# Performance work log

Hardware: AMD Instinct MI355X
Metric: run time of the kernel (lower is better)

Reference implementation:

```python
import jax, jax.numpy as jnp
import numpy as np

N_NODES = 100000
N_EDGES = 1600000
IN_F, HID_F, OUT_F = 64, 64, 64


def setup_inputs() -> dict:
    key = jax.random.key(0)
    ks = jax.random.split(key, 9)
    return {
        "x": jax.random.normal(ks[0], (N_NODES, IN_F), dtype=jnp.float32),
        "src": jax.random.randint(ks[1], (N_EDGES,), 0, N_NODES, dtype=jnp.int64),
        "dst": jax.random.randint(ks[2], (N_EDGES,), 0, N_NODES, dtype=jnp.int64),
        "W_self1": jax.random.normal(ks[3], (IN_F, HID_F), dtype=jnp.float32) * (1.0 / np.sqrt(IN_F)),
        "W_neigh1": jax.random.normal(ks[4], (IN_F, HID_F), dtype=jnp.float32) * (1.0 / np.sqrt(IN_F)),
        "b1": jnp.zeros((HID_F,), dtype=jnp.float32),
        "W_self2": jax.random.normal(ks[5], (HID_F, OUT_F), dtype=jnp.float32) * (1.0 / np.sqrt(HID_F)),
        "W_neigh2": jax.random.normal(ks[6], (HID_F, OUT_F), dtype=jnp.float32) * (1.0 / np.sqrt(HID_F)),
        "b2": jnp.zeros((OUT_F,), dtype=jnp.float32),
    }


def reference(x, src, dst, W_self1, W_neigh1, b1, W_self2, W_neigh2, b2):
    N = x.shape[0]
    # in-degree per destination node; zero-in-degree nodes get zero aggregate (DGL semantics)
    deg = jax.ops.segment_sum(jnp.ones(dst.shape, dtype=x.dtype), dst, num_segments=N)
    inv_deg = jnp.where(deg > 0, 1.0 / jnp.maximum(deg, 1.0), 0.0)[:, None]  # [N,1]

    def sage_conv(h, W_s, W_n, b):
        # mean over in-neighbors: gather src feats, segment-sum at dst, normalize
        agg = jax.ops.segment_sum(h[src], dst, num_segments=N) * inv_deg  # [N,F]
        return h @ W_s + agg @ W_n + b

    h = jax.nn.relu(sage_conv(x, W_self1, W_neigh1, b1))
    return sage_conv(h, W_self2, W_neigh2, b2)
```

## Files before the change

### kernel.cpp

```cpp
#include <hip/hip_runtime.h>

#define N_NODES 100000
#define N_EDGES 1600000
#define BKT 128
#define NBKT 782
#define BKT_SHIFT 7
#define BKT_MASK 127
#define DL_SHIFT 17
#define SRC_MASK 0x1FFFF
#define NT_TILES 6250
#define CNT_BLOCKS 128
#define CVT_BLOCKS 1563
#define ESRC_CAP 3072

typedef __attribute__((ext_vector_type(8))) short short8;
typedef __attribute__((ext_vector_type(4))) float float4v;

__device__ __forceinline__ unsigned short f2bf(float f) {
  unsigned u = __float_as_uint(f);
  return (unsigned short)((u + 0x7fffu + ((u >> 16) & 1u)) >> 16);
}
__device__ __forceinline__ float bflo(unsigned d) { return __uint_as_float(d << 16); }
__device__ __forceinline__ float bfhi(unsigned d) { return __uint_as_float(d & 0xffff0000u); }

__device__ __forceinline__ void acc_add(float a[8], uint4 v) {
  a[0] += bflo(v.x); a[1] += bfhi(v.x);
  a[2] += bflo(v.y); a[3] += bfhi(v.y);
  a[4] += bflo(v.z); a[5] += bfhi(v.z);
  a[6] += bflo(v.w); a[7] += bfhi(v.w);
}
__device__ __forceinline__ void acc_fma(float a[8], uint4 v, float m) {
  a[0] = fmaf(m, bflo(v.x), a[0]); a[1] = fmaf(m, bfhi(v.x), a[1]);
  a[2] = fmaf(m, bflo(v.y), a[2]); a[3] = fmaf(m, bfhi(v.y), a[3]);
  a[4] = fmaf(m, bflo(v.z), a[4]); a[5] = fmaf(m, bfhi(v.z), a[5]);
  a[6] = fmaf(m, bflo(v.w), a[6]); a[7] = fmaf(m, bfhi(v.w), a[7]);
}


__global__ void k_prep_count(const float* __restrict__ in, unsigned short* __restrict__ outb,
                             const float* __restrict__ W0, const float* __restrict__ W1,
                             const float* __restrict__ W2, const float* __restrict__ W3,
                             unsigned short* __restrict__ F,
                             const int* __restrict__ dst, int* __restrict__ blkCnt) {
  __shared__ int hist[NBKT];
  const int bid = blockIdx.x;
  if (bid < CNT_BLOCKS) {
    for (int t = threadIdx.x; t < NBKT; t += 256) hist[t] = 0;
    __syncthreads();
    const int e0 = bid * (N_EDGES / CNT_BLOCKS);
    const int e1 = e0 + (N_EDGES / CNT_BLOCKS);
    for (int e = e0 + threadIdx.x; e < e1; e += 256)
      atomicAdd(&hist[dst[e] >> BKT_SHIFT], 1);
    __syncthreads();
    for (int t = threadIdx.x; t < NBKT; t += 256)
      blkCnt[t * CNT_BLOCKS + bid] = hist[t];
    return;
  }
  if (bid < CNT_BLOCKS + 4) {
    if (threadIdx.x >= 64) return;
    const int wsel = bid - CNT_BLOCKS;
    const float* W = (wsel == 0) ? W0 : (wsel == 1) ? W1 : (wsel == 2) ? W2 : W3;
    unsigned short* out = F + wsel * 4096;
    int lane = threadIdx.x;
    int col = lane & 15, kr = lane >> 4;
    #pragma unroll
    for (int kc = 0; kc < 2; kc++)
      #pragma unroll
      for (int nt = 0; nt < 4; nt++) {
        unsigned d[4];
        #pragma unroll
        for (int jj = 0; jj < 4; jj++) {
          float w0 = W[(kc * 32 + kr * 8 + 2 * jj)     * 64 + nt * 16 + col];
          float w1 = W[(kc * 32 + kr * 8 + 2 * jj + 1) * 64 + nt * 16 + col];
          d[jj] = ((unsigned)f2bf(w1) << 16) | f2bf(w0);
        }
        uint4* p = (uint4*)(out + ((kc * 4 + nt) * 64 + lane) * 8);
        *p = make_uint4(d[0], d[1], d[2], d[3]);
      }
    return;
  }
  const int base = (bid - CNT_BLOCKS - 4) * 1024 + threadIdx.x;
  #pragma unroll
  for (int j = 0; j < 4; j++) {
    int i = base + j * 256;
    if (i < 1600000) {
      float4 v = ((const float4*)in)[i];
      unsigned d0 = ((unsigned)f2bf(v.y) << 16) | f2bf(v.x);
      unsigned d1 = ((unsigned)f2bf(v.w) << 16) | f2bf(v.z);
      ((uint2*)outb)[i] = make_uint2(d0, d1);
    }
  }
}


__global__ __launch_bounds__(512)
void k_scatter(const int* __restrict__ src, const int* __restrict__ dst,
               const int* __restrict__ blkCnt, int* __restrict__ bktStart,
               int* __restrict__ bktTot, int* __restrict__ binned) {
  __shared__ int totsh[NBKT];
  __shared__ int ps[NBKT];
  __shared__ int curb[NBKT];
  const int tid = threadIdx.x;
  const int bid = blockIdx.x;
  for (int t = tid; t < NBKT; t += 512) {
    const int* row = blkCnt + t * CNT_BLOCKS;
    int tot = 0, part = 0;
    #pragma unroll 4
    for (int i = 0; i < CNT_BLOCKS; i++) {
      int v = row[i];
      tot += v;
      if (i < bid) part += v;
    }
    totsh[t] = tot;
    curb[t] = part;
  }
  __syncthreads();
  if (tid < 64) {
    int running = 0;
    for (int base = 0; base < NBKT; base += 64) {
      int i = base + tid;
      int v = (i < NBKT) ? totsh[i] : 0;
      int inc = v;
      #pragma unroll
      for (int d = 1; d < 64; d <<= 1) { int y = __shfl_up(inc, d); if (tid >= d) inc += y; }
      if (i < NBKT) ps[i] = running + inc - v;
      running += __shfl(inc, 63);
    }
  }
  __syncthreads();
  for (int t = tid; t < NBKT; t += 512) curb[t] += ps[t];
  if (bid == 0)
    for (int t = tid; t < NBKT; t += 512) { bktStart[t] = ps[t]; bktTot[t] = totsh[t]; }
  __syncthreads();
  const int e0 = bid * (N_EDGES / CNT_BLOCKS);
  const int e1 = e0 + (N_EDGES / CNT_BLOCKS);
  for (int e = e0 + tid; e < e1; e += 512) {
    int d = dst[e];
    int s = src[e];
    int p = atomicAdd(&curb[d >> BKT_SHIFT], 1);
    binned[p] = s | ((d & BKT_MASK) << DL_SHIFT);
  }
}


__global__ __launch_bounds__(512)
void k_fused1(const unsigned short* __restrict__ featb, const int* __restrict__ binned,
              const int* __restrict__ bktStart, const int* __restrict__ bktTot,
              const unsigned short* __restrict__ wfS, const unsigned short* __restrict__ wfN,
              const float* __restrict__ bias,
              unsigned short* __restrict__ outb,
              int* __restrict__ off, int* __restrict__ esrc) {
  __shared__ int cnt[BKT];
  __shared__ int st[BKT];
  __shared__ int pos[BKT];
  __shared__ int wtot[2];
  __shared__ int esrc_l[ESRC_CAP];
  __shared__ unsigned short aggl[8][16 * 64];
  const int b = blockIdx.x;
  const int tid = threadIdx.x, lane = tid & 63;
  const int wv = tid >> 6;

  if (tid < BKT) cnt[tid] = 0;
  __syncthreads();
  const int s0 = bktStart[b], ne = bktTot[b];
  for (int i = tid; i < ne; i += 512)
    atomicAdd(&cnt[binned[s0 + i] >> DL_SHIFT], 1);
  __syncthreads();
  int c = 0, inc = 0;
  if (tid < BKT) {
    c = cnt[tid]; inc = c;
    #pragma unroll
    for (int d = 1; d < 64; d <<= 1) { int y = __shfl_up(inc, d); if (lane >= d) inc += y; }
    if (lane == 63) wtot[tid >> 6] = inc;
  }
  __syncthreads();
  if (tid < BKT) {
    int ex = inc - c + ((tid >= 64) ? wtot[0] : 0);
    st[tid] = ex; pos[tid] = ex;
    int n0 = (b << BKT_SHIFT) + tid;
    if (n0 < N_NODES) off[n0] = s0 + ex;
    if (n0 == N_NODES - 1) off[N_NODES] = N_EDGES;
  }
  __syncthreads();
  for (int i = tid; i < ne; i += 512) {
    int pe = binned[s0 + i];
    int p = atomicAdd(&pos[pe >> DL_SHIFT], 1);
    if (p < ESRC_CAP) esrc_l[p] = pe & SRC_MASK;
  }
  __syncthreads();
  for (int i = tid; i < ne; i += 512) esrc[s0 + i] = esrc_l[i];

  unsigned short* lw = &aggl[wv][0];
  const int n = lane >> 3;
  const int h = lane & 7;

  #pragma unroll
  for (int half = 0; half < 2; ++half) {
    const int row = half * 8 + n;
    const int lnode = wv * 16 + row;
    const int o0 = st[lnode];
    const int dg = cnt[lnode];
    const int o1 = o0 + dg;
    float a[8];
    #pragma unroll
    for (int q = 0; q < 8; q++) a[q] = 0.f;

    int i = o0;
    for (; i + 4 <= o1; i += 4) {
      int s0e = esrc_l[i], s1e = esrc_l[i + 1], s2e = esrc_l[i + 2], s3e = esrc_l[i + 3];
      uint4 v0 = *(const uint4*)(featb + s0e * 64 + h * 8);
      uint4 v1 = *(const uint4*)(featb + s1e * 64 + h * 8);
      uint4 v2 = *(const uint4*)(featb + s2e * 64 + h * 8);
      uint4 v3 = *(const uint4*)(featb + s3e * 64 + h * 8);
      acc_add(a, v0); acc_add(a, v1); acc_add(a, v2); acc_add(a, v3);
    }
    if (i < o1) {
      int last = o1 - 1;
      int e1 = min(i + 1, last), e2 = min(i + 2, last);
      float m1 = (i + 1 < o1) ? 1.f : 0.f;
      float m2 = (i + 2 < o1) ? 1.f : 0.f;
      int s0e = esrc_l[i], s1e = esrc_l[e1], s2e = esrc_l[e2];
      uint4 v0 = *(const uint4*)(featb + s0e * 64 + h * 8);
      uint4 v1 = *(const uint4*)(featb + s1e * 64 + h * 8);
      uint4 v2 = *(const uint4*)(featb + s2e * 64 + h * 8);
      acc_add(a, v0); acc_fma(a, v1, m1); acc_fma(a, v2, m2);
    }

    const float inv = (dg > 0) ? (1.0f / (float)dg) : 0.f;
    unsigned d0 = ((unsigned)f2bf(a[1] * inv) << 16) | f2bf(a[0] * inv);
    unsigned d1 = ((unsigned)f2bf(a[3] * inv) << 16) | f2bf(a[2] * inv);
    unsigned d2 = ((unsigned)f2bf(a[5] * inv) << 16) | f2bf(a[4] * inv);
    unsigned d3 = ((unsigned)f2bf(a[7] * inv) << 16) | f2bf(a[6] * inv);
    *(uint4*)(lw + row * 64 + ((h ^ (row & 7)) << 3)) = make_uint4(d0, d1, d2, d3);
  }

  __builtin_amdgcn_wave_barrier();
  asm volatile("" ::: "memory");

  const int tbase = (b << BKT_SHIFT) + wv * 16;
  if (tbase >= N_NODES) return;
  const int col = lane & 15, rr = lane >> 4;
  const int m = tbase + col;
  short8 as0 = *(const short8*)(featb + m * 64 + rr * 8);
  short8 as1 = *(const short8*)(featb + m * 64 + 32 + rr * 8);
  short8 aa0 = *(const short8*)(lw + col * 64 + ((rr ^ (col & 7)) << 3));
  short8 aa1 = *(const short8*)(lw + col * 64 + (((rr + 4) ^ (col & 7)) << 3));

  #pragma unroll
  for (int nt = 0; nt < 4; nt++) {
    short8 bs0 = *(const short8*)(wfS + ((0 * 4 + nt) * 64 + lane) * 8);
    short8 bs1 = *(const short8*)(wfS + ((1 * 4 + nt) * 64 + lane) * 8);
    short8 bn0 = *(const short8*)(wfN + ((0 * 4 + nt) * 64 + lane) * 8);
    short8 bn1 = *(const short8*)(wfN + ((1 * 4 + nt) * 64 + lane) * 8);
    float bvn = bias[nt * 16 + col];
    float4v cfr = {bvn, bvn, bvn, bvn};
    cfr = __builtin_amdgcn_mfma_f32_16x16x32_bf16(as0, bs0, cfr, 0, 0, 0);
    cfr = __builtin_amdgcn_mfma_f32_16x16x32_bf16(as1, bs1, cfr, 0, 0, 0);
    cfr = __builtin_amdgcn_mfma_f32_16x16x32_bf16(aa0, bn0, cfr, 0, 0, 0);
    cfr = __builtin_amdgcn_mfma_f32_16x16x32_bf16(aa1, bn1, cfr, 0, 0, 0);
    #pragma unroll
    for (int r2 = 0; r2 < 4; r2++) {
      int row = tbase + rr * 4 + r2;
      float v = fmaxf(cfr[r2], 0.f);
      outb[row * 64 + nt * 16 + col] = f2bf(v);
    }
  }
}


__global__ void k_fused2(const unsigned short* __restrict__ featb,
                         const int* __restrict__ off, const int* __restrict__ esrc,
                         const unsigned short* __restrict__ wfS,
                         const unsigned short* __restrict__ wfN,
                         const float* __restrict__ bias, float* __restrict__ outf) {
  __shared__ unsigned short aggl[4][16 * 64];
  const int tid = threadIdx.x;
  const int lane = tid & 63;
  const int wslot = tid >> 6;
  const int t = (blockIdx.x * blockDim.x + tid) >> 6;
  if (t >= NT_TILES) return;

  unsigned short* lw = &aggl[wslot][0];
  const int n = lane >> 3;
  const int h = lane & 7;

  #pragma unroll
  for (int half = 0; half < 2; ++half) {
    const int row = half * 8 + n;
    const int node = t * 16 + row;
    const int o0 = off[node];
    const int o1 = off[node + 1];
    float a[8];
    #pragma unroll
    for (int q = 0; q < 8; q++) a[q] = 0.f;

    int i = o0;
    for (; i + 4 <= o1; i += 4) {
      int s0 = esrc[i], s1 = esrc[i + 1], s2 = esrc[i + 2], s3 = esrc[i + 3];
      uint4 v0 = *(const uint4*)(featb + s0 * 64 + h * 8);
      uint4 v1 = *(const uint4*)(featb + s1 * 64 + h * 8);
      uint4 v2 = *(const uint4*)(featb + s2 * 64 + h * 8);
      uint4 v3 = *(const uint4*)(featb + s3 * 64 + h * 8);
      acc_add(a, v0); acc_add(a, v1); acc_add(a, v2); acc_add(a, v3);
    }
    if (i < o1) {
      int last = o1 - 1;
      int e1 = min(i + 1, last), e2 = min(i + 2, last);
      float m1 = (i + 1 < o1) ? 1.f : 0.f;
      float m2 = (i + 2 < o1) ? 1.f : 0.f;
      int s0 = esrc[i], s1 = esrc[e1], s2 = esrc[e2];
      uint4 v0 = *(const uint4*)(featb + s0 * 64 + h * 8);
      uint4 v1 = *(const uint4*)(featb + s1 * 64 + h * 8);
      uint4 v2 = *(const uint4*)(featb + s2 * 64 + h * 8);
      acc_add(a, v0); acc_fma(a, v1, m1); acc_fma(a, v2, m2);
    }

    const int dg = o1 - o0;
    const float inv = (dg > 0) ? (1.0f / (float)dg) : 0.f;
    unsigned d0 = ((unsigned)f2bf(a[1] * inv) << 16) | f2bf(a[0] * inv);
    unsigned d1 = ((unsigned)f2bf(a[3] * inv) << 16) | f2bf(a[2] * inv);
    unsigned d2 = ((unsigned)f2bf(a[5] * inv) << 16) | f2bf(a[4] * inv);
    unsigned d3 = ((unsigned)f2bf(a[7] * inv) << 16) | f2bf(a[6] * inv);
    *(uint4*)(lw + row * 64 + ((h ^ (row & 7)) << 3)) = make_uint4(d0, d1, d2, d3);
  }

  __builtin_amdgcn_wave_barrier();
  asm volatile("" ::: "memory");

  const int col = lane & 15, rr = lane >> 4;
  const int m = t * 16 + col;
  short8 as0 = *(const short8*)(featb + m * 64 + rr * 8);
  short8 as1 = *(const short8*)(featb + m * 64 + 32 + rr * 8);
  short8 aa0 = *(const short8*)(lw + col * 64 + ((rr ^ (col & 7)) << 3));
  short8 aa1 = *(const short8*)(lw + col * 64 + (((rr + 4) ^ (col & 7)) << 3));

  #pragma unroll
  for (int nt = 0; nt < 4; nt++) {
    short8 bs0 = *(const short8*)(wfS + ((0 * 4 + nt) * 64 + lane) * 8);
    short8 bs1 = *(const short8*)(wfS + ((1 * 4 + nt) * 64 + lane) * 8);
    short8 bn0 = *(const short8*)(wfN + ((0 * 4 + nt) * 64 + lane) * 8);
    short8 bn1 = *(const short8*)(wfN + ((1 * 4 + nt) * 64 + lane) * 8);
    float bvn = bias[nt * 16 + col];
    float4v cfr = {bvn, bvn, bvn, bvn};
    cfr = __builtin_amdgcn_mfma_f32_16x16x32_bf16(as0, bs0, cfr, 0, 0, 0);
    cfr = __builtin_amdgcn_mfma_f32_16x16x32_bf16(as1, bs1, cfr, 0, 0, 0);
    cfr = __builtin_amdgcn_mfma_f32_16x16x32_bf16(aa0, bn0, cfr, 0, 0, 0);
    cfr = __builtin_amdgcn_mfma_f32_16x16x32_bf16(aa1, bn1, cfr, 0, 0, 0);
    #pragma unroll
    for (int r2 = 0; r2 < 4; r2++) {
      int row = t * 16 + rr * 4 + r2;
      outf[row * 64 + nt * 16 + col] = cfr[r2];
    }
  }
}


extern "C" void kernel_launch(void* const* d_in, const int* in_sizes, int n_in,
                              void* d_out, int out_size, void* d_ws, size_t ws_size,
                              hipStream_t stream) {
  const float* x   = (const float*)d_in[0];
  const int*   src = (const int*)d_in[1];
  const int*   dst = (const int*)d_in[2];
  const float* Ws1 = (const float*)d_in[3];
  const float* Wn1 = (const float*)d_in[4];
  const float* b1  = (const float*)d_in[5];
  const float* Ws2 = (const float*)d_in[6];
  const float* Wn2 = (const float*)d_in[7];
  const float* b2  = (const float*)d_in[8];

  char* ws = (char*)d_ws;
  int*            blkCnt   = (int*)(ws + 0);
  int*            bktTot   = (int*)(ws + 400384);
  int*            bktStart = (int*)(ws + 403512);
  unsigned short* wf       = (unsigned short*)(ws + 406656);
  int*            off      = (int*)(ws + 439424);
  int*            binned   = (int*)(ws + 839680);
  int*            esrc     = (int*)(ws + 7239680);
  unsigned short* xbf      = (unsigned short*)(ws + 13639680);
  unsigned short* hbf      = (unsigned short*)(ws + 26439680);

  k_prep_count<<<CNT_BLOCKS + 4 + CVT_BLOCKS, 256, 0, stream>>>(
      x, xbf, Ws1, Wn1, Ws2, Wn2, wf, dst, blkCnt);
  k_scatter<<<CNT_BLOCKS, 512, 0, stream>>>(src, dst, blkCnt, bktStart, bktTot, binned);

  k_fused1<<<NBKT, 512, 0, stream>>>(xbf, binned, bktStart, bktTot,
                                     wf + 0 * 4096, wf + 1 * 4096, b1, hbf, off, esrc);
  k_fused2<<<1563, 256, 0, stream>>>(hbf, off, esrc, wf + 2 * 4096, wf + 3 * 4096,
                                     b2, (float*)d_out);
}
```

Before: 217.6 us.

## Add parallel bucket-count scan and reuse bucketed kernel for both layers

Raises the counting block count and moves the per-bucket prefix over block counts into a separate scan kernel, so the scatter kernel no longer loops serially over every block count per bucket. The second layer now reuses the bucketed fused kernel, which rebuilds the per-node edge ordering in shared memory from the binned array, instead of writing CSR offsets and esrc to global memory in layer one and reading them back. This trades an extra in-shared-memory counting sort in layer two for less global traffic and a simpler scatter, and adds one more kernel launch.

```diff
diff --git a/kernel.cpp b/kernel.cpp
--- a/kernel.cpp
+++ b/kernel.cpp
@@ -8,8 +8,7 @@
 #define BKT_MASK 127
 #define DL_SHIFT 17
 #define SRC_MASK 0x1FFFF
-#define NT_TILES 6250
-#define CNT_BLOCKS 128
+#define CNT_BLOCKS 256
 #define CVT_BLOCKS 1563
 #define ESRC_CAP 3072
 
@@ -93,33 +92,36 @@
 }
 
 
+__global__ void kA_scan1(int* __restrict__ blkCnt, int* __restrict__ bktTot) {
+  const int b = blockIdx.x;
+  const int tid = threadIdx.x, lane = tid & 63, w = tid >> 6;
+  __shared__ int wtot[4];
+  int v = blkCnt[b * CNT_BLOCKS + tid];
+  int inc = v;
+  #pragma unroll
+  for (int d = 1; d < 64; d <<= 1) { int y = __shfl_up(inc, d); if (lane >= d) inc += y; }
+  if (lane == 63) wtot[w] = inc;
+  __syncthreads();
+  int base = 0;
+  for (int j = 0; j < w; j++) base += wtot[j];
+  blkCnt[b * CNT_BLOCKS + tid] = base + inc - v;
+  if (tid == CNT_BLOCKS - 1) bktTot[b] = base + inc;
+}
+
+
 __global__ __launch_bounds__(512)
 void k_scatter(const int* __restrict__ src, const int* __restrict__ dst,
-               const int* __restrict__ blkCnt, int* __restrict__ bktStart,
-               int* __restrict__ bktTot, int* __restrict__ binned) {
-  __shared__ int totsh[NBKT];
+               const int* __restrict__ blkCnt, const int* __restrict__ bktTot,
+               int* __restrict__ bktStart, int* __restrict__ binned) {
   __shared__ int ps[NBKT];
   __shared__ int curb[NBKT];
   const int tid = threadIdx.x;
   const int bid = blockIdx.x;
-  for (int t = tid; t < NBKT; t += 512) {
-    const int* row = blkCnt + t * CNT_BLOCKS;
-    int tot = 0, part = 0;
-    #pragma unroll 4
-    for (int i = 0; i < CNT_BLOCKS; i++) {
-      int v = row[i];
-      tot += v;
-      if (i < bid) part += v;
-    }
-    totsh[t] = tot;
-    curb[t] = part;
-  }
-  __syncthreads();
   if (tid < 64) {
     int running = 0;
     for (int base = 0; base < NBKT; base += 64) {
       int i = base + tid;
-      int v = (i < NBKT) ? totsh[i] : 0;
+      int v = (i < NBKT) ? bktTot[i] : 0;
       int inc = v;
       #pragma unroll
       for (int d = 1; d < 64; d <<= 1) { int y = __shfl_up(inc, d); if (tid >= d) inc += y; }
@@ -128,9 +130,10 @@
     }
   }
   __syncthreads();
-  for (int t = tid; t < NBKT; t += 512) curb[t] += ps[t];
+  for (int t = tid; t < NBKT; t += 512)
+    curb[t] = ps[t] + blkCnt[t * CNT_BLOCKS + bid];
   if (bid == 0)
-    for (int t = tid; t < NBKT; t += 512) { bktStart[t] = ps[t]; bktTot[t] = totsh[t]; }
+    for (int t = tid; t < NBKT; t += 512) bktStart[t] = ps[t];
   __syncthreads();
   const int e0 = bid * (N_EDGES / CNT_BLOCKS);
   const int e1 = e0 + (N_EDGES / CNT_BLOCKS);
@@ -143,13 +146,13 @@
 }
 
 
+template <bool RELU, bool OUT_BF>
 __global__ __launch_bounds__(512)
-void k_fused1(const unsigned short* __restrict__ featb, const int* __restrict__ binned,
+void k_fusedB(const unsigned short* __restrict__ featb, const int* __restrict__ binned,
               const int* __restrict__ bktStart, const int* __restrict__ bktTot,
               const unsigned short* __restrict__ wfS, const unsigned short* __restrict__ wfN,
               const float* __restrict__ bias,
-              unsigned short* __restrict__ outb,
-              int* __restrict__ off, int* __restrict__ esrc) {
+              float* __restrict__ outf, unsigned short* __restrict__ outb) {
   __shared__ int cnt[BKT];
   __shared__ int st[BKT];
   __shared__ int pos[BKT];
@@ -177,9 +180,6 @@
   if (tid < BKT) {
     int ex = inc - c + ((tid >= 64) ? wtot[0] : 0);
     st[tid] = ex; pos[tid] = ex;
-    int n0 = (b << BKT_SHIFT) + tid;
-    if (n0 < N_NODES) off[n0] = s0 + ex;
-    if (n0 == N_NODES - 1) off[N_NODES] = N_EDGES;
   }
   __syncthreads();
   for (int i = tid; i < ne; i += 512) {
@@ -188,7 +188,6 @@
     if (p < ESRC_CAP) esrc_l[p] = pe & SRC_MASK;
   }
   __syncthreads();
-  for (int i = tid; i < ne; i += 512) esrc[s0 + i] = esrc_l[i];
 
   unsigned short* lw = &aggl[wv][0];
   const int n = lane >> 3;
@@ -261,95 +260,10 @@
     #pragma unroll
     for (int r2 = 0; r2 < 4; r2++) {
       int row = tbase + rr * 4 + r2;
-      float v = fmaxf(cfr[r2], 0.f);
-      outb[row * 64 + nt * 16 + col] = f2bf(v);
-    }
-  }
-}
-
-
-__global__ void k_fused2(const unsigned short* __restrict__ featb,
-                         const int* __restrict__ off, const int* __restrict__ esrc,
-                         const unsigned short* __restrict__ wfS,
-                         const unsigned short* __restrict__ wfN,
-                         const float* __restrict__ bias, float* __restrict__ outf) {
-  __shared__ unsigned short aggl[4][16 * 64];
-  const int tid = threadIdx.x;
-  const int lane = tid & 63;
-  const int wslot = tid >> 6;
-  const int t = (blockIdx.x * blockDim.x + tid) >> 6;
-  if (t >= NT_TILES) return;
-
-  unsigned short* lw = &aggl[wslot][0];
-  const int n = lane >> 3;
-  const int h = lane & 7;
-
-  #pragma unroll
-  for (int half = 0; half < 2; ++half) {
-    const int row = half * 8 + n;
-    const int node = t * 16 + row;
-    const int o0 = off[node];
-    const int o1 = off[node + 1];
-    float a[8];
-    #pragma unroll
-    for (int q = 0; q < 8; q++) a[q] = 0.f;
-
-    int i = o0;
-    for (; i + 4 <= o1; i += 4) {
-      int s0 = esrc[i], s1 = esrc[i + 1], s2 = esrc[i + 2], s3 = esrc[i + 3];
-      uint4 v0 = *(const uint4*)(featb + s0 * 64 + h * 8);
-      uint4 v1 = *(const uint4*)(featb + s1 * 64 + h * 8);
-      uint4 v2 = *(const uint4*)(featb + s2 * 64 + h * 8);
-      uint4 v3 = *(const uint4*)(featb + s3 * 64 + h * 8);
-      acc_add(a, v0); acc_add(a, v1); acc_add(a, v2); acc_add(a, v3);
-    }
-    if (i < o1) {
-      int last = o1 - 1;
-      int e1 = min(i + 1, last), e2 = min(i + 2, last);
-      float m1 = (i + 1 < o1) ? 1.f : 0.f;
-      float m2 = (i + 2 < o1) ? 1.f : 0.f;
-      int s0 = esrc[i], s1 = esrc[e1], s2 = esrc[e2];
-      uint4 v0 = *(const uint4*)(featb + s0 * 64 + h * 8);
-      uint4 v1 = *(const uint4*)(featb + s1 * 64 + h * 8);
-      uint4 v2 = *(const uint4*)(featb + s2 * 64 + h * 8);
-      acc_add(a, v0); acc_fma(a, v1, m1); acc_fma(a, v2, m2);
-    }
-
-    const int dg = o1 - o0;
-    const float inv = (dg > 0) ? (1.0f / (float)dg) : 0.f;
-    unsigned d0 = ((unsigned)f2bf(a[1] * inv) << 16) | f2bf(a[0] * inv);
-    unsigned d1 = ((unsigned)f2bf(a[3] * inv) << 16) | f2bf(a[2] * inv);
-    unsigned d2 = ((unsigned)f2bf(a[5] * inv) << 16) | f2bf(a[4] * inv);
-    unsigned d3 = ((unsigned)f2bf(a[7] * inv) << 16) | f2bf(a[6] * inv);
-    *(uint4*)(lw + row * 64 + ((h ^ (row & 7)) << 3)) = make_uint4(d0, d1, d2, d3);
-  }
-
-  __builtin_amdgcn_wave_barrier();
-  asm volatile("" ::: "memory");
-
-  const int col = lane & 15, rr = lane >> 4;
-  const int m = t * 16 + col;
-  short8 as0 = *(const short8*)(featb + m * 64 + rr * 8);
-  short8 as1 = *(const short8*)(featb + m * 64 + 32 + rr * 8);
-  short8 aa0 = *(const short8*)(lw + col * 64 + ((rr ^ (col & 7)) << 3));
-  short8 aa1 = *(const short8*)(lw + col * 64 + (((rr + 4) ^ (col & 7)) << 3));
-
-  #pragma unroll
-  for (int nt = 0; nt < 4; nt++) {
-    short8 bs0 = *(const short8*)(wfS + ((0 * 4 + nt) * 64 + lane) * 8);
-    short8 bs1 = *(const short8*)(wfS + ((1 * 4 + nt) * 64 + lane) * 8);
-    short8 bn0 = *(const short8*)(wfN + ((0 * 4 + nt) * 64 + lane) * 8);
-    short8 bn1 = *(const short8*)(wfN + ((1 * 4 + nt) * 64 + lane) * 8);
-    float bvn = bias[nt * 16 + col];
-    float4v cfr = {bvn, bvn, bvn, bvn};
-    cfr = __builtin_amdgcn_mfma_f32_16x16x32_bf16(as0, bs0, cfr, 0, 0, 0);
-    cfr = __builtin_amdgcn_mfma_f32_16x16x32_bf16(as1, bs1, cfr, 0, 0, 0);
-    cfr = __builtin_amdgcn_mfma_f32_16x16x32_bf16(aa0, bn0, cfr, 0, 0, 0);
-    cfr = __builtin_amdgcn_mfma_f32_16x16x32_bf16(aa1, bn1, cfr, 0, 0, 0);
-    #pragma unroll
-    for (int r2 = 0; r2 < 4; r2++) {
-      int row = t * 16 + rr * 4 + r2;
-      outf[row * 64 + nt * 16 + col] = cfr[r2];
+      float v = cfr[r2];
+      if (RELU) v = fmaxf(v, 0.f);
+      if (OUT_BF) outb[row * 64 + nt * 16 + col] = f2bf(v);
+      else        outf[row * 64 + nt * 16 + col] = v;
     }
   }
 }
@@ -370,21 +284,22 @@
 
   char* ws = (char*)d_ws;
   int*            blkCnt   = (int*)(ws + 0);
-  int*            bktTot   = (int*)(ws + 400384);
-  int*            bktStart = (int*)(ws + 403512);
-  unsigned short* wf       = (unsigned short*)(ws + 406656);
-  int*            off      = (int*)(ws + 439424);
-  int*            binned   = (int*)(ws + 839680);
-  int*            esrc     = (int*)(ws + 7239680);
-  unsigned short* xbf      = (unsigned short*)(ws + 13639680);
-  unsigned short* hbf      = (unsigned short*)(ws + 26439680);
+  int*            bktTot   = (int*)(ws + 800768);
+  int*            bktStart = (int*)(ws + 803896);
+  unsigned short* wf       = (unsigned short*)(ws + 807024);
+  int*            binned   = (int*)(ws + 839792);
+  unsigned short* xbf      = (unsigned short*)(ws + 7239792);
+  unsigned short* hbf      = (unsigned short*)(ws + 20039792);
 
   k_prep_count<<<CNT_BLOCKS + 4 + CVT_BLOCKS, 256, 0, stream>>>(
       x, xbf, Ws1, Wn1, Ws2, Wn2, wf, dst, blkCnt);
-  k_scatter<<<CNT_BLOCKS, 512, 0, stream>>>(src, dst, blkCnt, bktStart, bktTot, binned);
-
-  k_fused1<<<NBKT, 512, 0, stream>>>(xbf, binned, bktStart, bktTot,
-                                     wf + 0 * 4096, wf + 1 * 4096, b1, hbf, off, esrc);
-  k_fused2<<<1563, 256, 0, stream>>>(hbf, off, esrc, wf + 2 * 4096, wf + 3 * 4096,
-                                     b2, (float*)d_out);
-}
+  kA_scan1<<<NBKT, CNT_BLOCKS, 0, stream>>>(blkCnt, bktTot);
+  k_scatter<<<CNT_BLOCKS, 512, 0, stream>>>(src, dst, blkCnt, bktTot, bktStart, binned);
+
+  k_fusedB<true, true><<<NBKT, 512, 0, stream>>>(xbf, binned, bktStart, bktTot,
+                                                 wf + 0 * 4096, wf + 1 * 4096, b1,
+                                                 nullptr, hbf);
+  k_fusedB<false, false><<<NBKT, 512, 0, stream>>>(hbf, binned, bktStart, bktTot,
+                                                   wf + 2 * 4096, wf + 3 * 4096, b2,
+                                                   (float*)d_out, nullptr);
+}
```

Measured after the change: 232.3 us. 1.07x slower.
